# Kernel optimization log

Measured on AMD Instinct MI355X. Metric: run time of the kernel, lower is better.

Reference implementation:

```python
import jax, jax.numpy as jnp
import numpy as np

HIDDEN = 1152
HEADS = 16
HEAD_DIM = HIDDEN // HEADS

def setup_inputs() -> dict:
    key = jax.random.key(0)
    ks = jax.random.split(key, 7)
    s = 1.0 / np.sqrt(HIDDEN)
    return {
        "x": jax.random.normal(ks[0], (16, 1024, HIDDEN), dtype=jnp.float32),
        "w_qkv": jax.random.normal(ks[1], (3 * HIDDEN, HIDDEN), dtype=jnp.float32) * s,
        "b_qkv": jax.random.normal(ks[2], (3 * HIDDEN,), dtype=jnp.float32) * 0.01,
        "q_gamma": jnp.ones((HEAD_DIM,), dtype=jnp.float32),
        "k_gamma": jnp.ones((HEAD_DIM,), dtype=jnp.float32),
        "w_proj": jax.random.normal(ks[3], (HIDDEN, HIDDEN), dtype=jnp.float32) * s,
        "b_proj": jax.random.normal(ks[4], (HIDDEN,), dtype=jnp.float32) * 0.01,
    }

def _rmsnorm(t, gamma):
    # normalize over last dim (head_dim); torch RMSNorm default eps = finfo(dtype).eps
    eps = jnp.asarray(jnp.finfo(t.dtype).eps, t.dtype)
    ms = jnp.mean(jnp.square(t), axis=-1, keepdims=True)
    return t * jax.lax.rsqrt(ms + eps) * gamma

def reference(x, w_qkv, b_qkv, q_gamma, k_gamma, w_proj, b_proj):
    B, S, H = x.shape
    qkv = x @ w_qkv.T + b_qkv                       # [B,S,3H]
    qkv = qkv.reshape(B, S, 3, HEADS, HEAD_DIM)
    qkv = jnp.transpose(qkv, (2, 0, 3, 1, 4))       # [3,B,nh,S,hd]
    q, k, v = qkv[0], qkv[1], qkv[2]
    q = _rmsnorm(q, q_gamma)
    k = _rmsnorm(k, k_gamma)
    scale = 1.0 / np.sqrt(HEAD_DIM)
    scores = jnp.einsum('bhqd,bhkd->bhqk', q, k) * scale
    probs = jax.nn.softmax(scores, axis=-1)
    out = jnp.einsum('bhqk,bhkd->bhqd', probs, v)   # [B,nh,S,hd]
    out = jnp.transpose(out, (0, 2, 1, 3)).reshape(B, S, H)
    return out @ w_proj.T + b_proj
```

## Files before the change

### kernel.cpp

```cpp
#include <hip/hip_runtime.h>

typedef _Float16 f16;
typedef _Float16 f16x8 __attribute__((ext_vector_type(8)));
typedef _Float16 f16x4 __attribute__((ext_vector_type(4)));
typedef float f32x4 __attribute__((ext_vector_type(4)));

__device__ __forceinline__ void gld16(const void* g, void* l) {
    __builtin_amdgcn_global_load_lds(
        (const __attribute__((address_space(1))) void*)g,
        (__attribute__((address_space(3))) void*)l,
        16, 0, 0);
}

__global__ __launch_bounds__(256) void f32_to_f16_vec(const float* __restrict__ in,
                                                      f16* __restrict__ out, long n4) {
    long i = (long)blockIdx.x * 256 + threadIdx.x;
    if (i < n4) {
        float4 v = ((const float4*)in)[i];
        f16x4 o = {(f16)v.x, (f16)v.y, (f16)v.z, (f16)v.w};
        ((f16x4*)out)[i] = o;
    }
}

constexpr int GEMM_BUF_E = 12288;

template<int BUF, bool STG>
__device__ __forceinline__ void tile_step(f16* sm,
                                          const f16*& pA0, const f16*& pA1,
                                          const f16*& pB0,
                                          int dA0, int dA1, int dB0,
                                          int offA, int offB,
                                          f32x4 (&acc)[4][4]) {
    const f16* bp = sm + BUF * GEMM_BUF_E;
    f16x8 bf[4], af[2];
#pragma unroll
    for (int nt = 0; nt < 4; ++nt) bf[nt] = *(const f16x8*)(bp + offB + nt * 512);
#pragma unroll
    for (int mt = 0; mt < 2; ++mt) af[mt] = *(const f16x8*)(bp + offA + mt * 512);
    if (STG) {
        constexpr int SB = (BUF + 3) & 3;
        gld16(pA0, sm + SB * GEMM_BUF_E + dA0);
        gld16(pA1, sm + SB * GEMM_BUF_E + dA1);
    }
    __builtin_amdgcn_s_barrier();
    asm volatile("s_waitcnt lgkmcnt(0)" ::: "memory");
    __builtin_amdgcn_sched_barrier(0);
    __builtin_amdgcn_s_setprio(1);
#pragma unroll
    for (int mt = 0; mt < 2; ++mt)
#pragma unroll
        for (int nt = 0; nt < 4; ++nt)
            acc[mt][nt] = __builtin_amdgcn_mfma_f32_16x16x32_f16(
                af[mt], bf[nt], acc[mt][nt], 0, 0, 0);
    __builtin_amdgcn_s_setprio(0);
    __builtin_amdgcn_s_barrier();
    f16x8 ag[2];
#pragma unroll
    for (int mt = 0; mt < 2; ++mt) ag[mt] = *(const f16x8*)(bp + offA + 1024 + mt * 512);
    if (STG) {
        constexpr int SB = (BUF + 3) & 3;
        gld16(pB0, sm + SB * GEMM_BUF_E + dB0);
        pA0 += 32; pA1 += 32; pB0 += 32;
    }
    __builtin_amdgcn_s_barrier();
    asm volatile("s_waitcnt lgkmcnt(0)" ::: "memory");
    __builtin_amdgcn_sched_barrier(0);
    __builtin_amdgcn_s_setprio(1);
#pragma unroll
    for (int mt = 0; mt < 2; ++mt)
#pragma unroll
        for (int nt = 0; nt < 4; ++nt)
            acc[2 + mt][nt] = __builtin_amdgcn_mfma_f32_16x16x32_f16(
                ag[mt], bf[nt], acc[2 + mt][nt], 0, 0, 0);
    __builtin_amdgcn_s_setprio(0);
}

__global__ __launch_bounds__(512, 2) void gemm8(const f16* __restrict__ A,
                                                const f16* __restrict__ B,
                                                const float* __restrict__ bias,
                                                float* __restrict__ Cf,
                                                f16* __restrict__ Ch,
                                                int M, int N, int K) {
    __shared__ f16 sm[4 * GEMM_BUF_E];
    const int tid = threadIdx.x;
    const int w = tid >> 6, lane = tid & 63;
    const int quad = lane >> 4, l16 = lane & 15;
    const int wm = w >> 1, wn = w & 1;

    const int nnb = N >> 7;
    const int mpx = (M >> 8) >> 3;
    const int xcd = blockIdx.x & 7;
    const int s = blockIdx.x >> 3;
    const int mband = s / nnb;
    const int nblk = s - mband * nnb;
    const long m0 = (long)(xcd * mpx + mband) << 8;
    const long n0 = (long)nblk << 7;

    const int r4 = lane >> 2;
    const int sc = ((lane & 3) ^ ((lane >> 3) & 3)) << 3;
    const f16* gA0 = A + (m0 + w * 32 + r4) * (long)K + sc;
    const f16* gA1 = gA0 + (long)16 * K;
    const f16* gB0 = B + (n0 + w * 16 + r4) * (long)K + sc;
    const int dA0 = __builtin_amdgcn_readfirstlane(w * 1024);
    const int dA1 = dA0 + 512;
    const int dB0 = __builtin_amdgcn_readfirstlane(8192 + w * 512);

    const int swz = (quad ^ ((l16 >> 1) & 3)) << 3;
    const int offA = (wm * 64 + l16) * 32 + swz;
    const int offB = 8192 + (wn * 64 + l16) * 32 + swz;

    f32x4 acc[4][4] = {};

#pragma unroll
    for (int tt = 0; tt < 3; ++tt) {
        gld16(gA0 + tt * 32, sm + tt * GEMM_BUF_E + dA0);
        gld16(gA1 + tt * 32, sm + tt * GEMM_BUF_E + dA1);
        gld16(gB0 + tt * 32, sm + tt * GEMM_BUF_E + dB0);
    }
    const f16* pA0 = gA0 + 96;
    const f16* pA1 = gA1 + 96;
    const f16* pB0 = gB0 + 96;
    asm volatile("s_waitcnt vmcnt(6)" ::: "memory");
    __builtin_amdgcn_s_barrier();

#define VMB(NSTR) asm volatile("s_waitcnt vmcnt(" NSTR ")" ::: "memory"); \
                  __builtin_amdgcn_s_barrier();

#pragma unroll 1
    for (int it = 0; it < 8; ++it) {
        tile_step<0, true>(sm, pA0, pA1, pB0, dA0, dA1, dB0, offA, offB, acc); VMB("6")
        tile_step<1, true>(sm, pA0, pA1, pB0, dA0, dA1, dB0, offA, offB, acc); VMB("6")
        tile_step<2, true>(sm, pA0, pA1, pB0, dA0, dA1, dB0, offA, offB, acc); VMB("6")
        tile_step<3, true>(sm, pA0, pA1, pB0, dA0, dA1, dB0, offA, offB, acc); VMB("6")
    }
    tile_step<0, true >(sm, pA0, pA1, pB0, dA0, dA1, dB0, offA, offB, acc); VMB("6")
    tile_step<1, false>(sm, pA0, pA1, pB0, dA0, dA1, dB0, offA, offB, acc); VMB("3")
    tile_step<2, false>(sm, pA0, pA1, pB0, dA0, dA1, dB0, offA, offB, acc); VMB("0")
    tile_step<3, false>(sm, pA0, pA1, pB0, dA0, dA1, dB0, offA, offB, acc);
#undef VMB

    float bv[4];
#pragma unroll
    for (int nt = 0; nt < 4; ++nt)
        bv[nt] = bias ? bias[n0 + wn * 64 + nt * 16 + l16] : 0.f;
#pragma unroll
    for (int mt = 0; mt < 4; ++mt) {
#pragma unroll
        for (int r = 0; r < 4; ++r) {
            const long row = m0 + wm * 64 + mt * 16 + quad * 4 + r;
#pragma unroll
            for (int nt = 0; nt < 4; ++nt) {
                const long col = n0 + wn * 64 + nt * 16 + l16;
                const float v = acc[mt][nt][r] + bv[nt];
                if (Ch) Ch[row * (long)N + col] = (f16)v;
                else    Cf[row * (long)N + col] = v;
            }
        }
    }
}

__global__ __launch_bounds__(256) void qk_norm2(f16* __restrict__ qkv,
                                                const float* __restrict__ qg,
                                                const float* __restrict__ kg,
                                                f16* __restrict__ kc) {
    const float QSCALE = 0.117851130198f;
    const int t = blockIdx.x * 256 + threadIdx.x;
    const int h = t & 15;
    const long bs = t >> 4;
    f16* qp = qkv + bs * 3456 + h * 72;
    {
        f16x8 v[9];
        float ss = 0.f;
#pragma unroll
        for (int c = 0; c < 9; ++c) {
            v[c] = *(const f16x8*)(qp + c * 8);
#pragma unroll
            for (int j = 0; j < 8; ++j) { float f = (float)v[c][j]; ss += f * f; }
        }
        const float rs = rsqrtf(ss * (1.f / 72.f) + 1.1920928955078125e-7f) * QSCALE;
#pragma unroll
        for (int c = 0; c < 9; ++c) {
            f16x8 o;
#pragma unroll
            for (int j = 0; j < 8; ++j) o[j] = (f16)((float)v[c][j] * rs * qg[c * 8 + j]);
            *(f16x8*)(qp + c * 8) = o;
        }
    }
    {
        const f16* kp = qp + 1152;
        f16* dst = kc + ((long)((bs >> 10) * 16 + h) * 1024 + (bs & 1023)) * 72;
        f16x8 v[9];
        float ss = 0.f;
#pragma unroll
        for (int c = 0; c < 9; ++c) {
            v[c] = *(const f16x8*)(kp + c * 8);
#pragma unroll
            for (int j = 0; j < 8; ++j) { float f = (float)v[c][j]; ss += f * f; }
        }
        const float rs = rsqrtf(ss * (1.f / 72.f) + 1.1920928955078125e-7f);
#pragma unroll
        for (int c = 0; c < 9; ++c) {
            f16x8 o;
#pragma unroll
            for (int j = 0; j < 8; ++j) o[j] = (f16)((float)v[c][j] * rs * kg[c * 8 + j]);
            *(f16x8*)(dst + c * 8) = o;
        }
    }
}

__global__ __launch_bounds__(256) void vt_kernel(const f16* __restrict__ QKV,
                                                 f16* __restrict__ Vt) {
    __shared__ f16 tile[64][73];
    const int tid = threadIdx.x;
    const int bh = blockIdx.x;
    const int b = bh >> 4, h = bh & 15;
    const int s0 = blockIdx.y * 64;
    for (int idx = tid; idx < 64 * 72; idx += 256) {
        const int r = idx / 72, c = idx % 72;
        tile[r][c] = QKV[((long)(b * 1024 + s0 + r)) * 3456 + 2304 + h * 72 + c];
    }
    __syncthreads();
    for (int idx = tid; idx < 72 * 64; idx += 256) {
        const int d = idx >> 6, s = idx & 63;
        Vt[((long)bh * 72 + d) * 1024 + s0 + s] = tile[s][d];
    }
}

__global__ __launch_bounds__(256) void attn2(const f16* __restrict__ QKV,
                                             const f16* __restrict__ Kc,
                                             const f16* __restrict__ Vt,
                                             f16* __restrict__ O) {
    constexpr int S = 1024;
    __shared__ f16 smem[64 * 72 + 80 * 76];
    f16* Ks = smem;
    f16* Vs = smem + 64 * 72;
    const int tid = threadIdx.x;
    const int w = tid >> 6, lane = tid & 63;
    const int quad = lane >> 4, l16 = lane & 15;

    const int b = blockIdx.x;
    const int xcd = b & 7;
    const int j = b >> 3;
    const int bh = ((j >> 3) << 3) | xcd;
    const int qt = j & 7;
    const int bb = bh >> 4, h = bh & 15;
    const int q0 = qt * 128;

    for (int i = tid; i < 8 * 76; i += 256) {
        const int pr = i / 76, pc = i % 76;
        Vs[(72 + pr) * 76 + pc] = (pr == 0 && pc < 64) ? (f16)1.f : (f16)0.f;
    }

    const f16* qrow0 = QKV + ((long)(bb * 1024 + q0 + w * 32 + l16)) * 3456 + h * 72;
    const f16* qrow1 = qrow0 + (long)16 * 3456;
    f16x8 qz = {};
    f16x8 qf[2][3];
    qf[0][0] = *(const f16x8*)(qrow0 + quad * 8);
    qf[0][1] = *(const f16x8*)(qrow0 + 32 + quad * 8);
    qf[0][2] = (quad == 0) ? *(const f16x8*)(qrow0 + 64) : qz;
    qf[1][0] = *(const f16x8*)(qrow1 + quad * 8);
    qf[1][1] = *(const f16x8*)(qrow1 + 32 + quad * 8);
    qf[1][2] = (quad == 0) ? *(const f16x8*)(qrow1 + 64) : qz;

    f32x4 o[2][5] = {};

    const f16* gK = Kc + (long)bh * S * 72;
    const f16* gV = Vt + (long)bh * 72 * S;

    for (int s0 = 0; s0 < S; s0 += 64) {
        for (int ch = w; ch < 9; ch += 4)
            gld16(gK + (long)s0 * 72 + ch * 512 + lane * 8,
                  &Ks[__builtin_amdgcn_readfirstlane(ch * 512)]);
#pragma unroll
        for (int it = 0; it < 3; ++it) {
            const int idx = it * 256 + tid;
            if (idx < 576) {
                const int d = idx >> 3, s8 = (idx & 7) * 8;
                f16x8 v = *(const f16x8*)(gV + (long)d * 1024 + s0 + s8);
                f16x4 lo = {v[0], v[1], v[2], v[3]};
                f16x4 hi = {v[4], v[5], v[6], v[7]};
                *(f16x4*)&Vs[d * 76 + s8] = lo;
                *(f16x4*)&Vs[d * 76 + s8 + 4] = hi;
            }
        }
        __syncthreads();

        f32x4 sc[4][2] = {};
#pragma unroll
        for (int ss = 0; ss < 4; ++ss) {
            const int base = (ss * 16 + l16) * 72;
            f16x8 k0 = *(const f16x8*)&Ks[base + quad * 8];
            f16x8 k1 = *(const f16x8*)&Ks[base + 32 + quad * 8];
            f16x8 k2 = *(const f16x8*)&Ks[base + 64 + quad * 8];
            sc[ss][0] = __builtin_amdgcn_mfma_f32_16x16x32_f16(k0, qf[0][0], sc[ss][0], 0, 0, 0);
            sc[ss][0] = __builtin_amdgcn_mfma_f32_16x16x32_f16(k1, qf[0][1], sc[ss][0], 0, 0, 0);
            sc[ss][0] = __builtin_amdgcn_mfma_f32_16x16x32_f16(k2, qf[0][2], sc[ss][0], 0, 0, 0);
            sc[ss][1] = __builtin_amdgcn_mfma_f32_16x16x32_f16(k0, qf[1][0], sc[ss][1], 0, 0, 0);
            sc[ss][1] = __builtin_amdgcn_mfma_f32_16x16x32_f16(k1, qf[1][1], sc[ss][1], 0, 0, 0);
            sc[ss][1] = __builtin_amdgcn_mfma_f32_16x16x32_f16(k2, qf[1][2], sc[ss][1], 0, 0, 0);
        }

        f16x4 pf[4][2];
#pragma unroll
        for (int ss = 0; ss < 4; ++ss)
#pragma unroll
            for (int qs = 0; qs < 2; ++qs) {
                f16x4 pk;
#pragma unroll
                for (int r = 0; r < 4; ++r) pk[r] = (f16)__expf(sc[ss][qs][r]);
                pf[ss][qs] = pk;
            }

#pragma unroll
        for (int vt = 0; vt < 5; ++vt) {
#pragma unroll
            for (int ss = 0; ss < 4; ++ss) {
                f16x4 vf = *(const f16x4*)&Vs[(vt * 16 + l16) * 76 + ss * 16 + quad * 4];
                o[0][vt] = __builtin_amdgcn_mfma_f32_16x16x16f16(vf, pf[ss][0], o[0][vt], 0, 0, 0);
                o[1][vt] = __builtin_amdgcn_mfma_f32_16x16x16f16(vf, pf[ss][1], o[1][vt], 0, 0, 0);
            }
        }
        __syncthreads();
    }

    const float l0 = __shfl(o[0][4][0], 32 + l16);
    const float l1 = __shfl(o[1][4][0], 32 + l16);
    const float inv[2] = {1.f / l0, 1.f / l1};

    f16* es = smem + w * 2560;
#pragma unroll
    for (int qs = 0; qs < 2; ++qs) {
        f16* row = es + (qs * 16 + l16) * 80;
#pragma unroll
        for (int vt = 0; vt < 5; ++vt)
#pragma unroll
            for (int r = 0; r < 4; ++r) {
                const int d = vt * 16 + quad * 4 + r;
                if (d < 72) row[d] = (f16)(o[qs][vt][r] * inv[qs]);
            }
    }
    const long rowbase = (long)bb * 1024 + q0 + w * 32;
#pragma unroll
    for (int it = 0; it < 5; ++it) {
        const int idx = it * 64 + lane;
        if (idx < 288) {
            const int q = idx / 9, c = idx - q * 9;
            f16x4 a = *(const f16x4*)&es[q * 80 + c * 8];
            f16x4 b2 = *(const f16x4*)&es[q * 80 + c * 8 + 4];
            f16* dst = O + (rowbase + q) * 1152 + h * 72 + c * 8;
            *(f16x4*)dst = a;
            *(f16x4*)(dst + 4) = b2;
        }
    }
}

extern "C" void kernel_launch(void* const* d_in, const int* in_sizes, int n_in,
                              void* d_out, int out_size, void* d_ws, size_t ws_size,
                              hipStream_t stream) {
    const float* x       = (const float*)d_in[0];
    const float* w_qkv   = (const float*)d_in[1];
    const float* b_qkv   = (const float*)d_in[2];
    const float* q_gamma = (const float*)d_in[3];
    const float* k_gamma = (const float*)d_in[4];
    const float* w_proj  = (const float*)d_in[5];
    const float* b_proj  = (const float*)d_in[6];
    float* out = (float*)d_out;

    char* p = (char*)d_ws;
    f16* x_h = (f16*)p;      p += (size_t)16384 * 1152 * 2;
    f16* wqkv_h = (f16*)p;   p += (size_t)3456 * 1152 * 2;
    f16* wproj_h = (f16*)p;  p += (size_t)1152 * 1152 * 2;
    f16* qkv_h = (f16*)p;    p += (size_t)16384 * 3456 * 2;
    const size_t needed = (size_t)(p - (char*)d_ws);
    if (ws_size < needed) return;

    f16* k_c = (f16*)d_out;
    f16* v_t = (f16*)d_out + (size_t)16384 * 1152;

    f32_to_f16_vec<<<18432, 256, 0, stream>>>(x, x_h, 16384L * 1152 / 4);
    f32_to_f16_vec<<<3888, 256, 0, stream>>>(w_qkv, wqkv_h, 3456L * 1152 / 4);
    f32_to_f16_vec<<<1296, 256, 0, stream>>>(w_proj, wproj_h, 1152L * 1152 / 4);

    gemm8<<<1728, 512, 0, stream>>>(
        x_h, wqkv_h, b_qkv, nullptr, qkv_h, 16384, 3456, 1152);

    qk_norm2<<<1024, 256, 0, stream>>>(qkv_h, q_gamma, k_gamma, k_c);
    vt_kernel<<<dim3(256, 16), 256, 0, stream>>>(qkv_h, v_t);

    attn2<<<2048, 256, 0, stream>>>(qkv_h, k_c, v_t, x_h );

    gemm8<<<576, 512, 0, stream>>>(
        x_h, wproj_h, b_proj, out, nullptr, 16384, 1152, 1152);
}
```

Before: 554.4 us.

## Restructure GEMM to 4 waves with 128-row warp tiles and triple buffering

```diff
diff --git a/kernel.cpp b/kernel.cpp
--- a/kernel.cpp
+++ b/kernel.cpp
@@ -24,64 +24,61 @@
 
 constexpr int GEMM_BUF_E = 12288;
 
+struct GPtrs {
+    const f16 *a0, *a1, *a2, *a3, *b0, *b1;
+};
+
+__device__ __forceinline__ void stage6(f16* s, const GPtrs& g, int dA, int dB) {
+    gld16(g.a0, s + dA);
+    gld16(g.a1, s + dA + 2048);
+    gld16(g.a2, s + dA + 4096);
+    gld16(g.a3, s + dA + 6144);
+    gld16(g.b0, s + dB);
+    gld16(g.b1, s + dB + 2048);
+}
+
 template<int BUF, bool STG>
-__device__ __forceinline__ void tile_step(f16* sm,
-                                          const f16*& pA0, const f16*& pA1,
-                                          const f16*& pB0,
-                                          int dA0, int dA1, int dB0,
+__device__ __forceinline__ void tile_step(f16* sm, GPtrs& g,
+                                          int dA, int dB,
                                           int offA, int offB,
-                                          f32x4 (&acc)[4][4]) {
+                                          f32x4 (&acc)[8][4]) {
     const f16* bp = sm + BUF * GEMM_BUF_E;
-    f16x8 bf[4], af[2];
+    if (STG) {
+        constexpr int SB = (BUF + 2) % 3;
+        stage6(sm + SB * GEMM_BUF_E, g, dA, dB);
+        g.a0 += 32; g.a1 += 32; g.a2 += 32; g.a3 += 32;
+        g.b0 += 32; g.b1 += 32;
+    }
+    f16x8 bf[4], af[4], ag[4];
 #pragma unroll
     for (int nt = 0; nt < 4; ++nt) bf[nt] = *(const f16x8*)(bp + offB + nt * 512);
 #pragma unroll
-    for (int mt = 0; mt < 2; ++mt) af[mt] = *(const f16x8*)(bp + offA + mt * 512);
-    if (STG) {
-        constexpr int SB = (BUF + 3) & 3;
-        gld16(pA0, sm + SB * GEMM_BUF_E + dA0);
-        gld16(pA1, sm + SB * GEMM_BUF_E + dA1);
-    }
-    __builtin_amdgcn_s_barrier();
-    asm volatile("s_waitcnt lgkmcnt(0)" ::: "memory");
-    __builtin_amdgcn_sched_barrier(0);
+    for (int mt = 0; mt < 4; ++mt) af[mt] = *(const f16x8*)(bp + offA + mt * 512);
+#pragma unroll
+    for (int mt = 0; mt < 4; ++mt) ag[mt] = *(const f16x8*)(bp + offA + 2048 + mt * 512);
     __builtin_amdgcn_s_setprio(1);
 #pragma unroll
-    for (int mt = 0; mt < 2; ++mt)
+    for (int mt = 0; mt < 4; ++mt)
 #pragma unroll
         for (int nt = 0; nt < 4; ++nt)
             acc[mt][nt] = __builtin_amdgcn_mfma_f32_16x16x32_f16(
                 af[mt], bf[nt], acc[mt][nt], 0, 0, 0);
+#pragma unroll
+    for (int mt = 0; mt < 4; ++mt)
+#pragma unroll
+        for (int nt = 0; nt < 4; ++nt)
+            acc[4 + mt][nt] = __builtin_amdgcn_mfma_f32_16x16x32_f16(
+                ag[mt], bf[nt], acc[4 + mt][nt], 0, 0, 0);
     __builtin_amdgcn_s_setprio(0);
-    __builtin_amdgcn_s_barrier();
-    f16x8 ag[2];
-#pragma unroll
-    for (int mt = 0; mt < 2; ++mt) ag[mt] = *(const f16x8*)(bp + offA + 1024 + mt * 512);
-    if (STG) {
-        constexpr int SB = (BUF + 3) & 3;
-        gld16(pB0, sm + SB * GEMM_BUF_E + dB0);
-        pA0 += 32; pA1 += 32; pB0 += 32;
-    }
-    __builtin_amdgcn_s_barrier();
-    asm volatile("s_waitcnt lgkmcnt(0)" ::: "memory");
-    __builtin_amdgcn_sched_barrier(0);
-    __builtin_amdgcn_s_setprio(1);
-#pragma unroll
-    for (int mt = 0; mt < 2; ++mt)
-#pragma unroll
-        for (int nt = 0; nt < 4; ++nt)
-            acc[2 + mt][nt] = __builtin_amdgcn_mfma_f32_16x16x32_f16(
-                ag[mt], bf[nt], acc[2 + mt][nt], 0, 0, 0);
-    __builtin_amdgcn_s_setprio(0);
-}
-
-__global__ __launch_bounds__(512, 2) void gemm8(const f16* __restrict__ A,
+}
+
+__global__ __launch_bounds__(256, 2) void gemm8(const f16* __restrict__ A,
                                                 const f16* __restrict__ B,
                                                 const float* __restrict__ bias,
                                                 float* __restrict__ Cf,
                                                 f16* __restrict__ Ch,
                                                 int M, int N, int K) {
-    __shared__ f16 sm[4 * GEMM_BUF_E];
+    __shared__ f16 sm[3 * GEMM_BUF_E];
     const int tid = threadIdx.x;
     const int w = tid >> 6, lane = tid & 63;
     const int quad = lane >> 4, l16 = lane & 15;
@@ -98,45 +95,46 @@
 
     const int r4 = lane >> 2;
     const int sc = ((lane & 3) ^ ((lane >> 3) & 3)) << 3;
-    const f16* gA0 = A + (m0 + w * 32 + r4) * (long)K + sc;
-    const f16* gA1 = gA0 + (long)16 * K;
-    const f16* gB0 = B + (n0 + w * 16 + r4) * (long)K + sc;
-    const int dA0 = __builtin_amdgcn_readfirstlane(w * 1024);
-    const int dA1 = dA0 + 512;
-    const int dB0 = __builtin_amdgcn_readfirstlane(8192 + w * 512);
+    GPtrs g;
+    g.a0 = A + (m0 +   0 + w * 16 + r4) * (long)K + sc;
+    g.a1 = A + (m0 +  64 + w * 16 + r4) * (long)K + sc;
+    g.a2 = A + (m0 + 128 + w * 16 + r4) * (long)K + sc;
+    g.a3 = A + (m0 + 192 + w * 16 + r4) * (long)K + sc;
+    g.b0 = B + (n0 +   0 + w * 16 + r4) * (long)K + sc;
+    g.b1 = B + (n0 +  64 + w * 16 + r4) * (long)K + sc;
+    const int dA = __builtin_amdgcn_readfirstlane(w * 512);
+    const int dB = __builtin_amdgcn_readfirstlane(8192 + w * 512);
 
     const int swz = (quad ^ ((l16 >> 1) & 3)) << 3;
-    const int offA = (wm * 64 + l16) * 32 + swz;
+    const int offA = (wm * 128 + l16) * 32 + swz;
     const int offB = 8192 + (wn * 64 + l16) * 32 + swz;
 
-    f32x4 acc[4][4] = {};
-
-#pragma unroll
-    for (int tt = 0; tt < 3; ++tt) {
-        gld16(gA0 + tt * 32, sm + tt * GEMM_BUF_E + dA0);
-        gld16(gA1 + tt * 32, sm + tt * GEMM_BUF_E + dA1);
-        gld16(gB0 + tt * 32, sm + tt * GEMM_BUF_E + dB0);
-    }
-    const f16* pA0 = gA0 + 96;
-    const f16* pA1 = gA1 + 96;
-    const f16* pB0 = gB0 + 96;
+    f32x4 acc[8][4] = {};
+
+    stage6(sm, g, dA, dB);
+    {
+        GPtrs g1 = g;
+        g1.a0 += 32; g1.a1 += 32; g1.a2 += 32; g1.a3 += 32; g1.b0 += 32; g1.b1 += 32;
+        stage6(sm + GEMM_BUF_E, g1, dA, dB);
+    }
+    g.a0 += 64; g.a1 += 64; g.a2 += 64; g.a3 += 64; g.b0 += 64; g.b1 += 64;
     asm volatile("s_waitcnt vmcnt(6)" ::: "memory");
     __builtin_amdgcn_s_barrier();
+    __builtin_amdgcn_sched_barrier(0);
 
 #define VMB(NSTR) asm volatile("s_waitcnt vmcnt(" NSTR ")" ::: "memory"); \
-                  __builtin_amdgcn_s_barrier();
+                  __builtin_amdgcn_s_barrier();                           \
+                  __builtin_amdgcn_sched_barrier(0);
 
 #pragma unroll 1
-    for (int it = 0; it < 8; ++it) {
-        tile_step<0, true>(sm, pA0, pA1, pB0, dA0, dA1, dB0, offA, offB, acc); VMB("6")
-        tile_step<1, true>(sm, pA0, pA1, pB0, dA0, dA1, dB0, offA, offB, acc); VMB("6")
-        tile_step<2, true>(sm, pA0, pA1, pB0, dA0, dA1, dB0, offA, offB, acc); VMB("6")
-        tile_step<3, true>(sm, pA0, pA1, pB0, dA0, dA1, dB0, offA, offB, acc); VMB("6")
-    }
-    tile_step<0, true >(sm, pA0, pA1, pB0, dA0, dA1, dB0, offA, offB, acc); VMB("6")
-    tile_step<1, false>(sm, pA0, pA1, pB0, dA0, dA1, dB0, offA, offB, acc); VMB("3")
-    tile_step<2, false>(sm, pA0, pA1, pB0, dA0, dA1, dB0, offA, offB, acc); VMB("0")
-    tile_step<3, false>(sm, pA0, pA1, pB0, dA0, dA1, dB0, offA, offB, acc);
+    for (int it = 0; it < 11; ++it) {
+        tile_step<0, true>(sm, g, dA, dB, offA, offB, acc); VMB("6")
+        tile_step<1, true>(sm, g, dA, dB, offA, offB, acc); VMB("6")
+        tile_step<2, true>(sm, g, dA, dB, offA, offB, acc); VMB("6")
+    }
+    tile_step<0, true >(sm, g, dA, dB, offA, offB, acc); VMB("6")
+    tile_step<1, false>(sm, g, dA, dB, offA, offB, acc); VMB("0")
+    tile_step<2, false>(sm, g, dA, dB, offA, offB, acc);
 #undef VMB
 
     float bv[4];
@@ -144,10 +142,10 @@
     for (int nt = 0; nt < 4; ++nt)
         bv[nt] = bias ? bias[n0 + wn * 64 + nt * 16 + l16] : 0.f;
 #pragma unroll
-    for (int mt = 0; mt < 4; ++mt) {
+    for (int mt = 0; mt < 8; ++mt) {
 #pragma unroll
         for (int r = 0; r < 4; ++r) {
-            const long row = m0 + wm * 64 + mt * 16 + quad * 4 + r;
+            const long row = m0 + wm * 128 + mt * 16 + quad * 4 + r;
 #pragma unroll
             for (int nt = 0; nt < 4; ++nt) {
                 const long col = n0 + wn * 64 + nt * 16 + l16;
@@ -381,7 +379,7 @@
     f32_to_f16_vec<<<3888, 256, 0, stream>>>(w_qkv, wqkv_h, 3456L * 1152 / 4);
     f32_to_f16_vec<<<1296, 256, 0, stream>>>(w_proj, wproj_h, 1152L * 1152 / 4);
 
-    gemm8<<<1728, 512, 0, stream>>>(
+    gemm8<<<1728, 256, 0, stream>>>(
         x_h, wqkv_h, b_qkv, nullptr, qkv_h, 16384, 3456, 1152);
 
     qk_norm2<<<1024, 256, 0, stream>>>(qkv_h, q_gamma, k_gamma, k_c);
@@ -389,6 +387,6 @@
 
     attn2<<<2048, 256, 0, stream>>>(qkv_h, k_c, v_t, x_h );
 
-    gemm8<<<576, 512, 0, stream>>>(
+    gemm8<<<576, 256, 0, stream>>>(
         x_h, wproj_h, b_proj, out, nullptr, 16384, 1152, 1152);
 }
```

New measurement: 523.2 us. 5.6% less time.

## Restructure GEMM k-loop into two-phase double buffer with single MFMA burst per step

Applied to the files above, without the earlier changes.

```diff
diff --git a/kernel.cpp b/kernel.cpp
--- a/kernel.cpp
+++ b/kernel.cpp
@@ -22,56 +22,39 @@
     }
 }
 
-constexpr int GEMM_BUF_E = 12288;
-
-template<int BUF, bool STG>
-__device__ __forceinline__ void tile_step(f16* sm,
-                                          const f16*& pA0, const f16*& pA1,
-                                          const f16*& pB0,
-                                          int dA0, int dA1, int dB0,
-                                          int offA, int offB,
-                                          f32x4 (&acc)[4][4]) {
-    const f16* bp = sm + BUF * GEMM_BUF_E;
-    f16x8 bf[4], af[2];
-#pragma unroll
-    for (int nt = 0; nt < 4; ++nt) bf[nt] = *(const f16x8*)(bp + offB + nt * 512);
-#pragma unroll
-    for (int mt = 0; mt < 2; ++mt) af[mt] = *(const f16x8*)(bp + offA + mt * 512);
+constexpr int GBUF = 24576;
+
+template<int P, int KK, bool STG>
+__device__ __forceinline__ void phase_step(f16* sm,
+                                           const f16*& gSA, const f16*& gSB,
+                                           long sKA, int dA, int dB,
+                                           int rA, int rB,
+                                           f32x4 (&acc)[4][4]) {
+    const f16* ba = sm + P * GBUF + KK * 8192 + rA;
+    const f16* bb = sm + P * GBUF + KK * 4096 + rB;
+    f16x8 af[4], bf[4];
+#pragma unroll
+    for (int mt = 0; mt < 4; ++mt) af[mt] = *(const f16x8*)(ba + mt * 512);
+#pragma unroll
+    for (int nt = 0; nt < 4; ++nt) bf[nt] = *(const f16x8*)(bb + nt * 512);
     if (STG) {
-        constexpr int SB = (BUF + 3) & 3;
-        gld16(pA0, sm + SB * GEMM_BUF_E + dA0);
-        gld16(pA1, sm + SB * GEMM_BUF_E + dA1);
-    }
-    __builtin_amdgcn_s_barrier();
+        constexpr int TB = (KK == 0) ? (P ^ 1) : P;
+        constexpr int TK = (KK == 0) ? 1 : 0;
+        f16* d = sm + TB * GBUF;
+        gld16(gSA,       d + TK * 8192 + dA);
+        gld16(gSA + sKA, d + TK * 8192 + dA + 512);
+        gld16(gSB,       d + 16384 + TK * 4096 + dB);
+        gSA += 32; gSB += 32;
+    }
     asm volatile("s_waitcnt lgkmcnt(0)" ::: "memory");
     __builtin_amdgcn_sched_barrier(0);
     __builtin_amdgcn_s_setprio(1);
 #pragma unroll
-    for (int mt = 0; mt < 2; ++mt)
+    for (int mt = 0; mt < 4; ++mt)
 #pragma unroll
         for (int nt = 0; nt < 4; ++nt)
             acc[mt][nt] = __builtin_amdgcn_mfma_f32_16x16x32_f16(
                 af[mt], bf[nt], acc[mt][nt], 0, 0, 0);
-    __builtin_amdgcn_s_setprio(0);
-    __builtin_amdgcn_s_barrier();
-    f16x8 ag[2];
-#pragma unroll
-    for (int mt = 0; mt < 2; ++mt) ag[mt] = *(const f16x8*)(bp + offA + 1024 + mt * 512);
-    if (STG) {
-        constexpr int SB = (BUF + 3) & 3;
-        gld16(pB0, sm + SB * GEMM_BUF_E + dB0);
-        pA0 += 32; pA1 += 32; pB0 += 32;
-    }
-    __builtin_amdgcn_s_barrier();
-    asm volatile("s_waitcnt lgkmcnt(0)" ::: "memory");
-    __builtin_amdgcn_sched_barrier(0);
-    __builtin_amdgcn_s_setprio(1);
-#pragma unroll
-    for (int mt = 0; mt < 2; ++mt)
-#pragma unroll
-        for (int nt = 0; nt < 4; ++nt)
-            acc[2 + mt][nt] = __builtin_amdgcn_mfma_f32_16x16x32_f16(
-                ag[mt], bf[nt], acc[2 + mt][nt], 0, 0, 0);
     __builtin_amdgcn_s_setprio(0);
 }
 
@@ -81,7 +64,7 @@
                                                 float* __restrict__ Cf,
                                                 f16* __restrict__ Ch,
                                                 int M, int N, int K) {
-    __shared__ f16 sm[4 * GEMM_BUF_E];
+    __shared__ f16 sm[2 * GBUF];
     const int tid = threadIdx.x;
     const int w = tid >> 6, lane = tid & 63;
     const int quad = lane >> 4, l16 = lane & 15;
@@ -97,46 +80,42 @@
     const long n0 = (long)nblk << 7;
 
     const int r4 = lane >> 2;
-    const int sc = ((lane & 3) ^ ((lane >> 3) & 3)) << 3;
-    const f16* gA0 = A + (m0 + w * 32 + r4) * (long)K + sc;
-    const f16* gA1 = gA0 + (long)16 * K;
-    const f16* gB0 = B + (n0 + w * 16 + r4) * (long)K + sc;
-    const int dA0 = __builtin_amdgcn_readfirstlane(w * 1024);
-    const int dA1 = dA0 + 512;
-    const int dB0 = __builtin_amdgcn_readfirstlane(8192 + w * 512);
-
-    const int swz = (quad ^ ((l16 >> 1) & 3)) << 3;
-    const int offA = (wm * 64 + l16) * 32 + swz;
-    const int offB = 8192 + (wn * 64 + l16) * 32 + swz;
+    const int scw = ((lane & 3) ^ ((lane >> 3) & 3)) << 3;
+    const f16* gSA = A + (m0 + w * 32 + r4) * (long)K + scw;
+    const f16* gSB = B + (n0 + w * 16 + r4) * (long)K + scw;
+    const long sKA = (long)16 * K;
+    const int dA = __builtin_amdgcn_readfirstlane(w * 1024);
+    const int dB = __builtin_amdgcn_readfirstlane(w * 512);
+
+    const int swz8 = (quad ^ ((l16 >> 1) & 3)) << 3;
+    const int rA = (wm * 64 + l16) * 32 + swz8;
+    const int rB = 16384 + (wn * 64 + l16) * 32 + swz8;
 
     f32x4 acc[4][4] = {};
 
-#pragma unroll
-    for (int tt = 0; tt < 3; ++tt) {
-        gld16(gA0 + tt * 32, sm + tt * GEMM_BUF_E + dA0);
-        gld16(gA1 + tt * 32, sm + tt * GEMM_BUF_E + dA1);
-        gld16(gB0 + tt * 32, sm + tt * GEMM_BUF_E + dB0);
-    }
-    const f16* pA0 = gA0 + 96;
-    const f16* pA1 = gA1 + 96;
-    const f16* pB0 = gB0 + 96;
+    gld16(gSA, sm + dA); gld16(gSA + sKA, sm + dA + 512);
+    gld16(gSB, sm + 16384 + dB); gSA += 32; gSB += 32;
+    gld16(gSA, sm + 8192 + dA); gld16(gSA + sKA, sm + 8192 + dA + 512);
+    gld16(gSB, sm + 20480 + dB); gSA += 32; gSB += 32;
+    gld16(gSA, sm + GBUF + dA); gld16(gSA + sKA, sm + GBUF + dA + 512);
+    gld16(gSB, sm + GBUF + 16384 + dB); gSA += 32; gSB += 32;
     asm volatile("s_waitcnt vmcnt(6)" ::: "memory");
     __builtin_amdgcn_s_barrier();
 
-#define VMB(NSTR) asm volatile("s_waitcnt vmcnt(" NSTR ")" ::: "memory"); \
-                  __builtin_amdgcn_s_barrier();
+#define VMB(N) asm volatile("s_waitcnt vmcnt(" #N ")" ::: "memory"); \
+               __builtin_amdgcn_s_barrier();
 
 #pragma unroll 1
     for (int it = 0; it < 8; ++it) {
-        tile_step<0, true>(sm, pA0, pA1, pB0, dA0, dA1, dB0, offA, offB, acc); VMB("6")
-        tile_step<1, true>(sm, pA0, pA1, pB0, dA0, dA1, dB0, offA, offB, acc); VMB("6")
-        tile_step<2, true>(sm, pA0, pA1, pB0, dA0, dA1, dB0, offA, offB, acc); VMB("6")
-        tile_step<3, true>(sm, pA0, pA1, pB0, dA0, dA1, dB0, offA, offB, acc); VMB("6")
-    }
-    tile_step<0, true >(sm, pA0, pA1, pB0, dA0, dA1, dB0, offA, offB, acc); VMB("6")
-    tile_step<1, false>(sm, pA0, pA1, pB0, dA0, dA1, dB0, offA, offB, acc); VMB("3")
-    tile_step<2, false>(sm, pA0, pA1, pB0, dA0, dA1, dB0, offA, offB, acc); VMB("0")
-    tile_step<3, false>(sm, pA0, pA1, pB0, dA0, dA1, dB0, offA, offB, acc);
+        phase_step<0, 0, true>(sm, gSA, gSB, sKA, dA, dB, rA, rB, acc); VMB(6)
+        phase_step<0, 1, true>(sm, gSA, gSB, sKA, dA, dB, rA, rB, acc); VMB(6)
+        phase_step<1, 0, true>(sm, gSA, gSB, sKA, dA, dB, rA, rB, acc); VMB(6)
+        phase_step<1, 1, true>(sm, gSA, gSB, sKA, dA, dB, rA, rB, acc); VMB(6)
+    }
+    phase_step<0, 0, true >(sm, gSA, gSB, sKA, dA, dB, rA, rB, acc); VMB(6)
+    phase_step<0, 1, false>(sm, gSA, gSB, sKA, dA, dB, rA, rB, acc); VMB(3)
+    phase_step<1, 0, false>(sm, gSA, gSB, sKA, dA, dB, rA, rB, acc); VMB(0)
+    phase_step<1, 1, false>(sm, gSA, gSB, sKA, dA, dB, rA, rB, acc);
 #undef VMB
 
     float bv[4];
```

After: 528.0 us. 4.8% less time.
